# Kernel tuning notes

Measured on AMD Instinct MI355X. Metric: run time of the kernel, lower is better.

The kernel has to match this reference:

```python
import jax, jax.numpy as jnp
import numpy as np
from functools import partial

D_MODEL = 768
N_LAYER = 2
VOCAB = 50264  # 50257 padded to multiple of 8
D_STATE = 16
D_INNER = 2 * D_MODEL
DT_RANK = 48
D_CONV = 4
EPS = 1e-5
ZOH_EPS = 1e-7
B, L = 2, 1024


def setup_inputs() -> dict:
    key = jax.random.key(0)
    ks = jax.random.split(key, 16)
    s = 0.02
    inp = {
        'input_ids': jax.random.randint(ks[0], (B, L), 0, VOCAB, dtype=jnp.int32),
        'embedding': jax.random.normal(ks[1], (VOCAB, D_MODEL), jnp.float32) * s,
        'in_w': jax.random.normal(ks[2], (N_LAYER, D_MODEL, 2 * D_INNER), jnp.float32) * s,
        'in_b': jnp.zeros((N_LAYER, 2 * D_INNER), jnp.float32),
        'conv_w': jax.random.normal(ks[3], (N_LAYER, D_INNER, D_CONV), jnp.float32) * s,
        'conv_b': jnp.zeros((N_LAYER, D_INNER), jnp.float32),
        'xproj_w': jax.random.normal(ks[4], (N_LAYER, D_INNER, DT_RANK + 2 * D_STATE), jnp.float32) * s,
        'dt_w': jax.random.normal(ks[5], (N_LAYER, DT_RANK, D_INNER), jnp.float32) * s,
        'dt_b': jnp.zeros((N_LAYER, D_INNER), jnp.float32),
        'A_log': jnp.broadcast_to(jnp.log(jnp.arange(1, D_STATE + 1, dtype=jnp.float32))[None, None, :], (N_LAYER, D_INNER, D_STATE)).copy(),
        'Dp': jnp.ones((N_LAYER, D_INNER), jnp.float32),
        'out_w': jax.random.normal(ks[6], (N_LAYER, D_INNER, D_MODEL), jnp.float32) * s,
        'out_b': jnp.zeros((N_LAYER, D_MODEL), jnp.float32),
        'norm_w': jnp.ones((N_LAYER, D_MODEL), jnp.float32),
        'normf_w': jnp.ones((D_MODEL,), jnp.float32),
    }
    return inp


def rmsnorm(x, w):
    return x * jax.lax.rsqrt(jnp.mean(x * x, axis=-1, keepdims=True) + EPS) * w


def mamba_block(x, in_w, in_b, conv_w, conv_b, xproj_w, dt_w, dt_b, A_log, Dp, out_w, out_b):
    # x: (b, l, d_model)
    xr = x @ in_w + in_b                       # (b, l, 2*d_inner)
    xi, res = jnp.split(xr, 2, axis=-1)        # each (b, l, d_inner)
    # causal depthwise conv1d (torch pads d_conv-1 both sides then truncates to l)
    xc = jnp.transpose(xi, (0, 2, 1))          # (b, d_inner, l)
    xc = jax.lax.conv_general_dilated(
        xc, conv_w[:, None, :], (1,), [(D_CONV - 1, 0)],
        dimension_numbers=('NCH', 'OIH', 'NCH'), feature_group_count=D_INNER)
    xc = xc + conv_b[None, :, None]
    u = jax.nn.silu(jnp.transpose(xc, (0, 2, 1)))  # (b, l, d_inner)
    res = jax.nn.silu(res)
    # generate time-varying SSM params
    dbc = u @ xproj_w                          # (b, l, dt_rank + 2n)
    dt, Bm, Cm = jnp.split(dbc, [DT_RANK, DT_RANK + D_STATE], axis=-1)
    delta = jax.nn.softplus(dt @ dt_w + dt_b)  # (b, l, d_inner)
    A = -jnp.exp(A_log)                        # (d_inner, n)
    # ZOH discretization
    dA = jnp.exp(jnp.einsum('bld,dn->bldn', delta, A))            # (b,l,d_in,n)
    zoh = (dA - 1.0) / (A + ZOH_EPS)                               # (b,l,d_in,n)
    dBu = zoh * Bm[:, :, None, :] * u[..., None]                   # (b,l,d_in,n)
    # selective scan over l
    def step(s, inputs):
        dA_t, dBu_t, C_t = inputs              # (b,d_in,n),(b,d_in,n),(b,n)
        s = dA_t * s + dBu_t
        y = jnp.einsum('bdn,bn->bd', s, C_t)
        return s, y
    s0 = jnp.zeros((u.shape[0], D_INNER, D_STATE), u.dtype)
    _, ys = jax.lax.scan(step, s0, (jnp.moveaxis(dA, 1, 0), jnp.moveaxis(dBu, 1, 0), jnp.moveaxis(Cm, 1, 0)))
    y = jnp.moveaxis(ys, 0, 1) + u * Dp        # (b, l, d_inner)
    y = y * res
    return y @ out_w + out_b


def forward(input_ids, embedding, in_w, in_b, conv_w, conv_b, xproj_w, dt_w, dt_b, A_log, Dp, out_w, out_b, norm_w, normf_w):
    x = embedding[input_ids]                   # (b, l, d_model)
    for i in range(N_LAYER):
        mixed = mamba_block(x, in_w[i], in_b[i], conv_w[i], conv_b[i], xproj_w[i],
                            dt_w[i], dt_b[i], A_log[i], Dp[i], out_w[i], out_b[i])
        x = rmsnorm(mixed + x, norm_w[i])      # ResidualBlock: norm(mixer(x)+x)
    x = rmsnorm(x, normf_w)
    return x @ embedding.T                     # tied lm_head, (b, l, vocab)


def reference(input_ids, embedding, in_w, in_b, conv_w, conv_b, xproj_w, dt_w, dt_b, A_log, Dp, out_w, out_b, norm_w, normf_w):
    return forward(input_ids, embedding, in_w, in_b, conv_w, conv_b, xproj_w,
                   dt_w, dt_b, A_log, Dp, out_w, out_b, norm_w, normf_w)
```

## Files before the change

kernel.cpp:

```cpp
#include <hip/hip_runtime.h>
#include <math.h>
#include <stdint.h>

#define BB 2
#define LL 1024
#define DM 768
#define NL 2
#define VV 50264
#define VP2 50432
#define DS 16
#define DI 1536
#define DR 48
#define DC 4
#define MM (BB*LL)

#define CH 32
#define NC (LL/CH)

#define KS 8

#define TS 64
#define KT 16

typedef __attribute__((ext_vector_type(8))) short short8;
typedef __attribute__((ext_vector_type(4))) float f32x4;

#define AS3(p) ((__attribute__((address_space(3))) unsigned int*)(unsigned int)(uintptr_t)(p))
#define AS1(p) ((const __attribute__((address_space(1))) unsigned int*)(uintptr_t)(p))

__device__ __forceinline__ unsigned short f2bf(float v) {
    union { float f; unsigned u; } x; x.f = v;
    unsigned r = x.u + 0x7fffu + ((x.u >> 16) & 1u);
    return (unsigned short)(r >> 16);
}

__global__ __launch_bounds__(256) void embed_kernel(
    const int* __restrict__ ids, const float* __restrict__ emb,
    float* __restrict__ x, unsigned short* __restrict__ x16)
{
    int m = blockIdx.x;
    int v = ids[m];
    const float* src = emb + (size_t)v * DM;
    float* dst = x + (size_t)m * DM;
    unsigned short* dst16 = x16 + (size_t)m * DM;
    for (int i = threadIdx.x; i < DM; i += 256) {
        float f = src[i];
        dst[i] = f;
        dst16[i] = f2bf(f);
    }
}

__global__ __launch_bounds__(256) void emb_convert_kernel(
    const float* __restrict__ emb, unsigned short* __restrict__ out)
{
    size_t i8 = (size_t)blockIdx.x * 256 + threadIdx.x;
    size_t row = i8 / 96;
    size_t col8 = (i8 - row * 96) * 8;
    if (row >= VP2) return;
    ushort4 o0, o1;
    if (row < VV) {
        const float* p = emb + row * DM + col8;
        float4 v0 = *(const float4*)p;
        float4 v1 = *(const float4*)(p + 4);
        o0.x = f2bf(v0.x); o0.y = f2bf(v0.y); o0.z = f2bf(v0.z); o0.w = f2bf(v0.w);
        o1.x = f2bf(v1.x); o1.y = f2bf(v1.y); o1.z = f2bf(v1.z); o1.w = f2bf(v1.w);
    } else {
        o0 = make_ushort4(0, 0, 0, 0);
        o1 = o0;
    }
    unsigned short* op = out + row * DM + col8;
    *(ushort4*)op = o0;
    *(ushort4*)(op + 4) = o1;
}

__global__ __launch_bounds__(256) void transpose_bf16_kernel(
    const float* __restrict__ in, unsigned short* __restrict__ out, int R, int C)
{
    __shared__ float t[32][33];
    int l = blockIdx.z;
    int r0 = blockIdx.y * 32, c0 = blockIdx.x * 32;
    int tx = threadIdx.x & 31, ty = threadIdx.x >> 5;
    const float* ip = in + (size_t)l * R * C;
    unsigned short* op = out + (size_t)l * C * R;
    #pragma unroll
    for (int j = 0; j < 32; j += 8)
        t[ty + j][tx] = ip[(size_t)(r0 + ty + j) * C + c0 + tx];
    __syncthreads();
    #pragma unroll
    for (int j = 0; j < 32; j += 8)
        op[(size_t)(c0 + ty + j) * R + r0 + tx] = f2bf(t[tx][ty + j]);
}

__global__ __launch_bounds__(256) void gemm_mfma_bt(
    const unsigned short* __restrict__ A, const unsigned short* __restrict__ B,
    const float* __restrict__ bias, const float* __restrict__ resid,
    float* __restrict__ C, int M, int N, int K, int MT, int NTILES)
{
    int T = MT * NTILES;
    int q = T >> 3, r = T & 7;
    int orig = blockIdx.x;
    int xcd = orig & 7, u = orig >> 3;
    int wg = (xcd < r ? xcd * (q + 1) : r * (q + 1) + (xcd - r) * q) + u;
    int mt = wg % MT, nt = wg / MT;

    __shared__ unsigned short As[3][128 * 32];
    __shared__ unsigned short Bs[3][128 * 32];
    int tid = threadIdx.x;
    int w = tid >> 6, lane = tid & 63;
    int m0 = mt * 128, n0 = nt * 128;

    int rA = lane >> 2;
    int kb = (lane & 3) * 8;
    const unsigned short* gA0 = A + (size_t)(m0 + w * 16 + rA) * K + kb;
    const unsigned short* gA1 = gA0 + (size_t)64 * K;
    const unsigned short* gB0 = B + (size_t)(n0 + w * 16 + rA) * K + kb;
    const unsigned short* gB1 = gB0 + (size_t)64 * K;

    int lr = lane & 15, lk = lane >> 4;
    int wr = (w >> 1) * 64, wc = (w & 1) * 64;

    f32x4 acc[4][4] = {};

#define STAGE(k0, buf) do { \
    __builtin_amdgcn_global_load_lds(AS1(gA0 + (k0)), AS3(&As[buf][(w * 16) * 32]), 16, 0, 0); \
    __builtin_amdgcn_global_load_lds(AS1(gA1 + (k0)), AS3(&As[buf][(64 + w * 16) * 32]), 16, 0, 0); \
    __builtin_amdgcn_global_load_lds(AS1(gB0 + (k0)), AS3(&Bs[buf][(w * 16) * 32]), 16, 0, 0); \
    __builtin_amdgcn_global_load_lds(AS1(gB1 + (k0)), AS3(&Bs[buf][(64 + w * 16) * 32]), 16, 0, 0); \
} while (0)

#define COMPUTE(buf) do { \
    short8 a[4], b[4]; \
    _Pragma("unroll") \
    for (int f = 0; f < 4; ++f) \
        a[f] = *(const short8*)&As[buf][(wr + f * 16 + lr) * 32 + lk * 8]; \
    _Pragma("unroll") \
    for (int f = 0; f < 4; ++f) \
        b[f] = *(const short8*)&Bs[buf][(wc + f * 16 + lr) * 32 + lk * 8]; \
    _Pragma("unroll") \
    for (int i = 0; i < 4; ++i) \
        _Pragma("unroll") \
        for (int j = 0; j < 4; ++j) \
            acc[i][j] = __builtin_amdgcn_mfma_f32_16x16x32_bf16(a[i], b[j], acc[i][j], 0, 0, 0); \
} while (0)

    int nsteps = K / 32;
    STAGE(0, 0);
    STAGE(32, 1);
    asm volatile("s_waitcnt vmcnt(4)" ::: "memory");
    __builtin_amdgcn_s_barrier();
    __builtin_amdgcn_sched_barrier(0);

    for (int t = 0; t < nsteps; ++t) {
        int cur = t % 3;
        if (t + 2 < nsteps)
            STAGE((t + 2) * 32, (t + 2) % 3);
        COMPUTE(cur);
        if (t + 1 < nsteps) {
            if (t + 2 < nsteps)
                asm volatile("s_waitcnt vmcnt(4)" ::: "memory");
            else
                asm volatile("s_waitcnt vmcnt(0)" ::: "memory");
            __builtin_amdgcn_s_barrier();
            __builtin_amdgcn_sched_barrier(0);
        }
    }

#undef STAGE
#undef COMPUTE

    #pragma unroll
    for (int i = 0; i < 4; ++i) {
        int row = m0 + wr + i * 16 + lk * 4;
        #pragma unroll
        for (int j = 0; j < 4; ++j) {
            int col = n0 + wc + j * 16 + lr;
            if (col < N) {
                float bv = bias ? bias[col] : 0.f;
                #pragma unroll
                for (int r2 = 0; r2 < 4; ++r2) {
                    float v = acc[i][j][r2] + bv;
                    if (resid) v += resid[(size_t)(row + r2) * N + col];
                    C[(size_t)(row + r2) * N + col] = v;
                }
            }
        }
    }
}

__global__ __launch_bounds__(512) void gemm_mfma_256(
    const unsigned short* __restrict__ A, const unsigned short* __restrict__ B,
    float* __restrict__ C, int M, int N, int K, int MT, int NTILES)
{
    int T = MT * NTILES;
    int q = T >> 3, r = T & 7;
    int orig = blockIdx.x;
    int xcd = orig & 7, u = orig >> 3;
    int wg = (xcd < r ? xcd * (q + 1) : r * (q + 1) + (xcd - r) * q) + u;
    int mt = wg % MT, nt = wg / MT;

    __shared__ unsigned short As[3][256 * 32];
    __shared__ unsigned short Bs[3][256 * 32];
    int tid = threadIdx.x;
    int w = tid >> 6, lane = tid & 63;
    int wm = w >> 2, wn = w & 3;
    int m0 = mt * 256, n0 = nt * 256;

    int srow = tid >> 2;
    int schunk = (tid & 3) ^ ((srow & 3) ^ ((srow >> 2) & 3));
    const unsigned short* gA0 = A + (size_t)(m0 + srow) * K + schunk * 8;
    const unsigned short* gA1 = gA0 + (size_t)128 * K;
    const unsigned short* gB0 = B + (size_t)(n0 + srow) * K + schunk * 8;
    const unsigned short* gB1 = gB0 + (size_t)128 * K;

    int lr = lane & 15, lk = lane >> 4;
    int rc = (lk ^ ((lr & 3) ^ ((lr >> 2) & 3))) * 8;

    f32x4 acc[8][4] = {};

#define STAGE_A(k0, buf) do { \
    __builtin_amdgcn_global_load_lds(AS1(gA0 + (k0)), AS3(&As[buf][(w * 16) * 32]), 16, 0, 0); \
    __builtin_amdgcn_global_load_lds(AS1(gA1 + (k0)), AS3(&As[buf][(128 + w * 16) * 32]), 16, 0, 0); \
} while (0)
#define STAGE_B(k0, buf) do { \
    __builtin_amdgcn_global_load_lds(AS1(gB0 + (k0)), AS3(&Bs[buf][(w * 16) * 32]), 16, 0, 0); \
    __builtin_amdgcn_global_load_lds(AS1(gB1 + (k0)), AS3(&Bs[buf][(128 + w * 16) * 32]), 16, 0, 0); \
} while (0)

    int nsteps = K / 32;

    STAGE_A(0, 0); STAGE_B(0, 0);
    STAGE_A(32, 1); STAGE_B(32, 1);
    asm volatile("s_waitcnt vmcnt(4)" ::: "memory");
    __builtin_amdgcn_s_barrier();
    __builtin_amdgcn_sched_barrier(0);

    for (int t = 0; t < nsteps; ++t) {
        int s = t % 3;
        int sn = (t + 2) % 3;
        bool stage2 = (t + 2) < nsteps;
        short8 av[4], bv[4];

        #pragma unroll
        for (int f = 0; f < 4; ++f)
            av[f] = *(const short8*)&As[s][(wm * 128 + f * 16 + lr) * 32 + rc];
        #pragma unroll
        for (int f = 0; f < 4; ++f)
            bv[f] = *(const short8*)&Bs[s][(wn * 64 + f * 16 + lr) * 32 + rc];
        if (stage2) STAGE_A((t + 2) * 32, sn);
        __builtin_amdgcn_s_barrier();
        asm volatile("s_waitcnt lgkmcnt(0)" ::: "memory");
        __builtin_amdgcn_sched_barrier(0);
        __builtin_amdgcn_s_setprio(1);
        #pragma unroll
        for (int i = 0; i < 4; ++i)
            #pragma unroll
            for (int j = 0; j < 4; ++j)
                acc[i][j] = __builtin_amdgcn_mfma_f32_16x16x32_bf16(av[i], bv[j], acc[i][j], 0, 0, 0);
        __builtin_amdgcn_s_setprio(0);
        __builtin_amdgcn_s_barrier();

        #pragma unroll
        for (int f = 0; f < 4; ++f)
            av[f] = *(const short8*)&As[s][(wm * 128 + (4 + f) * 16 + lr) * 32 + rc];
        if (stage2) STAGE_B((t + 2) * 32, sn);
        __builtin_amdgcn_s_barrier();
        asm volatile("s_waitcnt lgkmcnt(0)" ::: "memory");
        __builtin_amdgcn_sched_barrier(0);
        __builtin_amdgcn_s_setprio(1);
        #pragma unroll
        for (int i = 0; i < 4; ++i)
            #pragma unroll
            for (int j = 0; j < 4; ++j)
                acc[4 + i][j] = __builtin_amdgcn_mfma_f32_16x16x32_bf16(av[i], bv[j], acc[4 + i][j], 0, 0, 0);
        __builtin_amdgcn_s_setprio(0);

        if (t + 1 < nsteps) {
            if (stage2)
                asm volatile("s_waitcnt vmcnt(4)" ::: "memory");
            else
                asm volatile("s_waitcnt vmcnt(0)" ::: "memory");
            __builtin_amdgcn_s_barrier();
            __builtin_amdgcn_sched_barrier(0);
        }
    }

#undef STAGE_A
#undef STAGE_B

    #pragma unroll
    for (int i = 0; i < 8; ++i) {
        int row = m0 + wm * 128 + i * 16 + lk * 4;
        #pragma unroll
        for (int j = 0; j < 4; ++j) {
            int col = n0 + wn * 64 + j * 16 + lr;
            if (col < N) {
                #pragma unroll
                for (int r2 = 0; r2 < 4; ++r2)
                    C[(size_t)(row + r2) * N + col] = acc[i][j][r2];
            }
        }
    }
}

template<int ACT>
__global__ __launch_bounds__(256) void gemm_tiled(
    const float* __restrict__ A, const float* __restrict__ Bm,
    const float* __restrict__ bias, float* __restrict__ C,
    int M, int N, int K, int lda)
{
    __shared__ float As[KT][TS + 4];
    __shared__ float Bs[KT][TS + 4];
    int tid = threadIdx.x;
    int tx = tid & 15, ty = tid >> 4;
    int m0 = blockIdx.y * TS;
    int n0 = blockIdx.x * TS;
    float acc[4][4] = {};

    for (int k0 = 0; k0 < K; k0 += KT) {
        {
            int i = tid >> 2;
            int k4 = (tid & 3) * 4;
            int m = m0 + i;
            float4 v = make_float4(0.f, 0.f, 0.f, 0.f);
            if (m < M) v = *(const float4*)(A + (size_t)m * lda + k0 + k4);
            As[k4 + 0][i] = v.x; As[k4 + 1][i] = v.y;
            As[k4 + 2][i] = v.z; As[k4 + 3][i] = v.w;
        }
        {
            int k = tid >> 4;
            int j4 = (tid & 15) * 4;
            int n = n0 + j4;
            float4 v = make_float4(0.f, 0.f, 0.f, 0.f);
            const float* p = Bm + (size_t)(k0 + k) * N + n;
            if (n + 3 < N) {
                v = *(const float4*)p;
            } else {
                float t0 = (n + 0 < N) ? p[0] : 0.f;
                float t1 = (n + 1 < N) ? p[1] : 0.f;
                float t2 = (n + 2 < N) ? p[2] : 0.f;
                float t3 = (n + 3 < N) ? p[3] : 0.f;
                v = make_float4(t0, t1, t2, t3);
            }
            Bs[k][j4 + 0] = v.x; Bs[k][j4 + 1] = v.y;
            Bs[k][j4 + 2] = v.z; Bs[k][j4 + 3] = v.w;
        }
        __syncthreads();
        #pragma unroll
        for (int k = 0; k < KT; ++k) {
            float a[4], b[4];
            #pragma unroll
            for (int q2 = 0; q2 < 4; ++q2) a[q2] = As[k][ty * 4 + q2];
            #pragma unroll
            for (int q2 = 0; q2 < 4; ++q2) b[q2] = Bs[k][tx * 4 + q2];
            #pragma unroll
            for (int i = 0; i < 4; ++i)
                #pragma unroll
                for (int j = 0; j < 4; ++j)
                    acc[i][j] = fmaf(a[i], b[j], acc[i][j]);
        }
        __syncthreads();
    }

    #pragma unroll
    for (int i = 0; i < 4; ++i) {
        int m = m0 + ty * 4 + i;
        if (m >= M) continue;
        #pragma unroll
        for (int j = 0; j < 4; ++j) {
            int n = n0 + tx * 4 + j;
            if (n >= N) continue;
            float v = acc[i][j];
            if (bias)  v += bias[n];
            if (ACT == 1) v = fmaxf(v, 0.f) + log1pf(expf(-fabsf(v)));
            C[(size_t)m * N + n] = v;
        }
    }
}

__global__ __launch_bounds__(256) void xproj_part_kernel(
    const float* __restrict__ A, const float* __restrict__ Bm, float* __restrict__ part)
{
    __shared__ float As[KT][TS + 4];
    __shared__ float Bs[KT][TS + 4];
    int tid = threadIdx.x;
    int tx = tid & 15, ty = tid >> 4;
    int m0 = blockIdx.y * TS;
    int n0 = blockIdx.x * TS;
    int kbeg = blockIdx.z * (DI / KS);
    const int N = 80;
    float acc[4][4] = {};

    for (int k0 = kbeg; k0 < kbeg + DI / KS; k0 += KT) {
        {
            int i = tid >> 2;
            int k4 = (tid & 3) * 4;
            float4 v = *(const float4*)(A + (size_t)(m0 + i) * DI + k0 + k4);
            As[k4 + 0][i] = v.x; As[k4 + 1][i] = v.y;
            As[k4 + 2][i] = v.z; As[k4 + 3][i] = v.w;
        }
        {
            int k = tid >> 4;
            int j4 = (tid & 15) * 4;
            int n = n0 + j4;
            const float* p = Bm + (size_t)(k0 + k) * N + n;
            float4 v;
            if (n + 3 < N) {
                v = *(const float4*)p;
            } else {
                v.x = (n + 0 < N) ? p[0] : 0.f;
                v.y = (n + 1 < N) ? p[1] : 0.f;
                v.z = (n + 2 < N) ? p[2] : 0.f;
                v.w = (n + 3 < N) ? p[3] : 0.f;
            }
            Bs[k][j4 + 0] = v.x; Bs[k][j4 + 1] = v.y;
            Bs[k][j4 + 2] = v.z; Bs[k][j4 + 3] = v.w;
        }
        __syncthreads();
        #pragma unroll
        for (int k = 0; k < KT; ++k) {
            float a[4], b[4];
            #pragma unroll
            for (int q2 = 0; q2 < 4; ++q2) a[q2] = As[k][ty * 4 + q2];
            #pragma unroll
            for (int q2 = 0; q2 < 4; ++q2) b[q2] = Bs[k][tx * 4 + q2];
            #pragma unroll
            for (int i = 0; i < 4; ++i)
                #pragma unroll
                for (int j = 0; j < 4; ++j)
                    acc[i][j] = fmaf(a[i], b[j], acc[i][j]);
        }
        __syncthreads();
    }

    float* op = part + (size_t)blockIdx.z * MM * 80;
    #pragma unroll
    for (int i = 0; i < 4; ++i) {
        int m = m0 + ty * 4 + i;
        #pragma unroll
        for (int j = 0; j < 4; ++j) {
            int n = n0 + tx * 4 + j;
            if (n < 80) op[(size_t)m * 80 + n] = acc[i][j];
        }
    }
}

__global__ __launch_bounds__(256) void xproj_reduce_kernel(
    const float* __restrict__ part, float* __restrict__ dbc)
{
    int i = blockIdx.x * 256 + threadIdx.x;
    if (i >= MM * 80) return;
    float s = 0.f;
    #pragma unroll
    for (int z = 0; z < KS; ++z) s += part[(size_t)z * MM * 80 + i];
    dbc[i] = s;
}

__global__ __launch_bounds__(256) void conv_silu_kernel(
    const float* __restrict__ xr, const float* __restrict__ cw,
    const float* __restrict__ cb, float* __restrict__ u)
{
    int d = blockIdx.x * 256 + threadIdx.x;
    int l = blockIdx.y;
    int b = blockIdx.z;
    float acc = cb[d];
    #pragma unroll
    for (int j = 0; j < DC; ++j) {
        int lp = l - (DC - 1) + j;
        if (lp >= 0)
            acc = fmaf(xr[((size_t)(b * LL + lp)) * (2 * DI) + d], cw[d * DC + j], acc);
    }
    float s = acc / (1.f + expf(-acc));
    u[((size_t)(b * LL + l)) * DI + d] = s;
}

__global__ __launch_bounds__(256) void scan_reduce_kernel(
    const float* __restrict__ delta, const float* __restrict__ u,
    const float* __restrict__ dbc, const float* __restrict__ A_log,
    float* __restrict__ P, float* __restrict__ Q)
{
    int d = blockIdx.x * 256 + threadIdx.x;
    int c = blockIdx.y;
    int b = blockIdx.z;

    float Av[DS], invA[DS];
    {
        const float4* ap = (const float4*)(A_log + (size_t)d * DS);
        #pragma unroll
        for (int n4 = 0; n4 < 4; ++n4) {
            float4 a = ap[n4];
            Av[n4 * 4 + 0] = -expf(a.x); Av[n4 * 4 + 1] = -expf(a.y);
            Av[n4 * 4 + 2] = -expf(a.z); Av[n4 * 4 + 3] = -expf(a.w);
        }
        #pragma unroll
        for (int n = 0; n < DS; ++n) invA[n] = 1.f / (Av[n] + 1e-7f);
    }

    float p[DS], s[DS];
    #pragma unroll
    for (int n = 0; n < DS; ++n) { p[n] = 1.f; s[n] = 0.f; }

    const float* dp = delta + ((size_t)b * LL + c * CH) * DI + d;
    const float* up = u     + ((size_t)b * LL + c * CH) * DI + d;
    const float* bb = dbc   + ((size_t)b * LL + c * CH) * 80 + DR;

    for (int l = 0; l < CH; ++l) {
        float dlt = dp[(size_t)l * DI];
        float uv  = up[(size_t)l * DI];
        float Bv[DS];
        {
            const float4* bp4 = (const float4*)(bb + (size_t)l * 80);
            #pragma unroll
            for (int n4 = 0; n4 < 4; ++n4) {
                float4 v = bp4[n4];
                Bv[n4 * 4 + 0] = v.x; Bv[n4 * 4 + 1] = v.y;
                Bv[n4 * 4 + 2] = v.z; Bv[n4 * 4 + 3] = v.w;
            }
        }
        #pragma unroll
        for (int n = 0; n < DS; ++n) {
            float dA = expf(dlt * Av[n]);
            float dBu = (dA - 1.f) * invA[n] * Bv[n] * uv;
            p[n] *= dA;
            s[n] = fmaf(dA, s[n], dBu);
        }
    }

    float* Pp = P + (((size_t)b * NC + c) * DI + d) * DS;
    float* Qp = Q + (((size_t)b * NC + c) * DI + d) * DS;
    #pragma unroll
    for (int n4 = 0; n4 < 4; ++n4) {
        ((float4*)Pp)[n4] = make_float4(p[n4 * 4 + 0], p[n4 * 4 + 1], p[n4 * 4 + 2], p[n4 * 4 + 3]);
        ((float4*)Qp)[n4] = make_float4(s[n4 * 4 + 0], s[n4 * 4 + 1], s[n4 * 4 + 2], s[n4 * 4 + 3]);
    }
}

__global__ __launch_bounds__(256) void scan_apply_kernel(
    const float* __restrict__ delta, const float* __restrict__ u,
    const float* __restrict__ dbc, const float* __restrict__ xr,
    const float* __restrict__ A_log, const float* __restrict__ Dp,
    const float* __restrict__ P, const float* __restrict__ Q,
    unsigned short* __restrict__ y16)
{
    int d = blockIdx.x * 256 + threadIdx.x;
    int c = blockIdx.y;
    int b = blockIdx.z;

    float Av[DS], invA[DS];
    {
        const float4* ap = (const float4*)(A_log + (size_t)d * DS);
        #pragma unroll
        for (int n4 = 0; n4 < 4; ++n4) {
            float4 a = ap[n4];
            Av[n4 * 4 + 0] = -expf(a.x); Av[n4 * 4 + 1] = -expf(a.y);
            Av[n4 * 4 + 2] = -expf(a.z); Av[n4 * 4 + 3] = -expf(a.w);
        }
        #pragma unroll
        for (int n = 0; n < DS; ++n) invA[n] = 1.f / (Av[n] + 1e-7f);
    }
    float Dv = Dp[d];

    float s[DS];
    #pragma unroll
    for (int n = 0; n < DS; ++n) s[n] = 0.f;
    for (int cc = 0; cc < c; ++cc) {
        const float* Pp = P + (((size_t)b * NC + cc) * DI + d) * DS;
        const float* Qp = Q + (((size_t)b * NC + cc) * DI + d) * DS;
        float pv[DS], qv[DS];
        #pragma unroll
        for (int n4 = 0; n4 < 4; ++n4) {
            float4 pw = ((const float4*)Pp)[n4];
            float4 qw = ((const float4*)Qp)[n4];
            pv[n4 * 4 + 0] = pw.x; pv[n4 * 4 + 1] = pw.y; pv[n4 * 4 + 2] = pw.z; pv[n4 * 4 + 3] = pw.w;
            qv[n4 * 4 + 0] = qw.x; qv[n4 * 4 + 1] = qw.y; qv[n4 * 4 + 2] = qw.z; qv[n4 * 4 + 3] = qw.w;
        }
        #pragma unroll
        for (int n = 0; n < DS; ++n) s[n] = fmaf(pv[n], s[n], qv[n]);
    }

    const float* dp = delta + ((size_t)b * LL + c * CH) * DI + d;
    const float* up = u     + ((size_t)b * LL + c * CH) * DI + d;
    const float* xp = xr    + ((size_t)b * LL + c * CH) * (2 * DI) + DI + d;
    const float* bb = dbc   + ((size_t)b * LL + c * CH) * 80 + DR;
    unsigned short* yp = y16 + ((size_t)b * LL + c * CH) * DI + d;

    for (int l = 0; l < CH; ++l) {
        float dlt = dp[(size_t)l * DI];
        float uv  = up[(size_t)l * DI];
        float rv  = xp[(size_t)l * (2 * DI)];
        float Bv[DS], Cv[DS];
        {
            const float4* bp4 = (const float4*)(bb + (size_t)l * 80);
            #pragma unroll
            for (int n4 = 0; n4 < 4; ++n4) {
                float4 v = bp4[n4];
                Bv[n4 * 4 + 0] = v.x; Bv[n4 * 4 + 1] = v.y;
                Bv[n4 * 4 + 2] = v.z; Bv[n4 * 4 + 3] = v.w;
            }
            #pragma unroll
            for (int n4 = 0; n4 < 4; ++n4) {
                float4 v = bp4[4 + n4];
                Cv[n4 * 4 + 0] = v.x; Cv[n4 * 4 + 1] = v.y;
                Cv[n4 * 4 + 2] = v.z; Cv[n4 * 4 + 3] = v.w;
            }
        }
        float pv = 0.f;
        #pragma unroll
        for (int n = 0; n < DS; ++n) {
            float dA = expf(dlt * Av[n]);
            float dBu = (dA - 1.f) * invA[n] * Bv[n] * uv;
            s[n] = fmaf(dA, s[n], dBu);
            pv = fmaf(s[n], Cv[n], pv);
        }
        float res = rv / (1.f + expf(-rv));
        yp[(size_t)l * DI] = f2bf((pv + uv * Dv) * res);
    }
}

__global__ __launch_bounds__(256) void rmsnorm_kernel(
    const float* __restrict__ in, const float* __restrict__ w,
    float* __restrict__ outf, unsigned short* __restrict__ outb)
{
    int m = blockIdx.x;
    const float* row = in + (size_t)m * DM;
    float ss = 0.f;
    for (int i = threadIdx.x; i < DM; i += 256) { float v = row[i]; ss = fmaf(v, v, ss); }
    #pragma unroll
    for (int off = 32; off > 0; off >>= 1) ss += __shfl_down(ss, off);
    __shared__ float sred[4];
    __shared__ float sscale;
    int wid = threadIdx.x >> 6;
    if ((threadIdx.x & 63) == 0) sred[wid] = ss;
    __syncthreads();
    if (threadIdx.x == 0) {
        float tot = sred[0] + sred[1] + sred[2] + sred[3];
        sscale = 1.f / sqrtf(tot / (float)DM + 1e-5f);
    }
    __syncthreads();
    float sc = sscale;
    for (int i = threadIdx.x; i < DM; i += 256) {
        float v = row[i] * sc * w[i];
        if (outf) outf[(size_t)m * DM + i] = v;
        if (outb) outb[(size_t)m * DM + i] = f2bf(v);
    }
}

extern "C" void kernel_launch(void* const* d_in, const int* in_sizes, int n_in,
                              void* d_out, int out_size, void* d_ws, size_t ws_size,
                              hipStream_t stream)
{
    const int*   ids      = (const int*)  d_in[0];
    const float* emb      = (const float*)d_in[1];
    const float* in_w     = (const float*)d_in[2];
    const float* in_b     = (const float*)d_in[3];
    const float* conv_w   = (const float*)d_in[4];
    const float* conv_b   = (const float*)d_in[5];
    const float* xproj_w  = (const float*)d_in[6];
    const float* dt_w     = (const float*)d_in[7];
    const float* dt_b     = (const float*)d_in[8];
    const float* A_log    = (const float*)d_in[9];
    const float* Dp       = (const float*)d_in[10];
    const float* out_w    = (const float*)d_in[11];
    const float* out_b    = (const float*)d_in[12];
    const float* norm_w   = (const float*)d_in[13];
    const float* normf_w  = (const float*)d_in[14];
    float* out = (float*)d_out;

    char* wsp = (char*)d_ws;
    auto alloc = [&](size_t bytes) {
        char* p = wsp;
        wsp += (bytes + 255) & ~(size_t)255;
        return p;
    };
    float* x     = (float*)alloc((size_t)MM * DM * 4);
    float* xr    = (float*)alloc((size_t)MM * 2 * DI * 4);
    float* u     = (float*)alloc((size_t)MM * DI * 4);
    float* dbc   = (float*)alloc((size_t)MM * 80 * 4);
    float* part  = (float*)alloc((size_t)KS * MM * 80 * 4);
    float* delta = (float*)alloc((size_t)MM * DI * 4);
    float* tmp   = (float*)alloc((size_t)MM * DM * 4);
    float* Pbuf  = (float*)alloc((size_t)BB * NC * DI * DS * 4);
    float* Qbuf  = (float*)alloc((size_t)BB * NC * DI * DS * 4);
    unsigned short* x16     = (unsigned short*)alloc((size_t)MM * DM * 2);
    unsigned short* y16     = (unsigned short*)alloc((size_t)MM * DI * 2);
    unsigned short* emb16   = (unsigned short*)alloc((size_t)VP2 * DM * 2);
    unsigned short* in_wT   = (unsigned short*)alloc((size_t)NL * 2 * DI * DM * 2);
    unsigned short* out_wT  = (unsigned short*)alloc((size_t)NL * DM * DI * 2);

    emb_convert_kernel<<<((size_t)VP2 * (DM / 8) + 255) / 256, 256, 0, stream>>>(emb, emb16);
    transpose_bf16_kernel<<<dim3(2 * DI / 32, DM / 32, NL), 256, 0, stream>>>(
        in_w, in_wT, DM, 2 * DI);
    transpose_bf16_kernel<<<dim3(DM / 32, DI / 32, NL), 256, 0, stream>>>(
        out_w, out_wT, DI, DM);

    embed_kernel<<<MM, 256, 0, stream>>>(ids, emb, x, x16);

    for (int layer = 0; layer < NL; ++layer) {
        const float* lb_in  = in_b    + (size_t)layer * 2 * DI;
        const float* lcw    = conv_w  + (size_t)layer * DI * DC;
        const float* lcb    = conv_b  + (size_t)layer * DI;
        const float* lxw    = xproj_w + (size_t)layer * DI * (DR + 2 * DS);
        const float* ldtw   = dt_w    + (size_t)layer * DR * DI;
        const float* ldtb   = dt_b    + (size_t)layer * DI;
        const float* lAlog  = A_log   + (size_t)layer * DI * DS;
        const float* lDp    = Dp      + (size_t)layer * DI;
        const float* lob    = out_b   + (size_t)layer * DM;
        const float* lnw    = norm_w  + (size_t)layer * DM;
        const unsigned short* lw_inT = in_wT  + (size_t)layer * 2 * DI * DM;
        const unsigned short* lw_outT= out_wT + (size_t)layer * DM * DI;

        gemm_mfma_bt<<<16 * 24, 256, 0, stream>>>(
            x16, lw_inT, lb_in, nullptr, xr, MM, 2 * DI, DM, 16, 24);

        conv_silu_kernel<<<dim3(DI / 256, LL, BB), 256, 0, stream>>>(xr, lcw, lcb, u);

        xproj_part_kernel<<<dim3(2, MM / TS, KS), 256, 0, stream>>>(u, lxw, part);
        xproj_reduce_kernel<<<(MM * 80 + 255) / 256, 256, 0, stream>>>(part, dbc);

        gemm_tiled<1><<<dim3(DI / TS, MM / TS), 256, 0, stream>>>(
            dbc, ldtw, ldtb, delta, MM, DI, DR, DR + 2 * DS);

        scan_reduce_kernel<<<dim3(DI / 256, NC, BB), 256, 0, stream>>>(
            delta, u, dbc, lAlog, Pbuf, Qbuf);
        scan_apply_kernel<<<dim3(DI / 256, NC, BB), 256, 0, stream>>>(
            delta, u, dbc, xr, lAlog, lDp, Pbuf, Qbuf, y16);

        gemm_mfma_bt<<<16 * 6, 256, 0, stream>>>(
            y16, lw_outT, lob, x, tmp, MM, DM, DI, 16, 6);

        rmsnorm_kernel<<<MM, 256, 0, stream>>>(tmp, lnw, x, x16);
    }

    rmsnorm_kernel<<<MM, 256, 0, stream>>>(x, normf_w, nullptr, x16);

    gemm_mfma_256<<<8 * (VP2 / 256), 512, 0, stream>>>(
        x16, emb16, out, MM, VV, DM, 8, VP2 / 256);
}
```

Before: 810.9 us.

## Fuse fp32-to-bf16 embedding conversion into lm_head GEMM B-operand staging

Removes the separate emb_convert_kernel that wrote a full bf16 copy of the embedding table. The lm_head GEMM now loads fp32 embedding rows into registers, converts them to bf16 and writes them into swizzled shared memory itself, and loads for later steps are issued ahead so they overlap the MFMA work. This saves one full pass over the 154MB table plus the bf16 write and re-read. In exchange, each of the 8 M-tiles re-reads and re-converts fp32 B (twice the bytes of bf16), and the register-staged path replaces the direct global-to-LDS loads, which may weaken pipelining.

```diff
diff --git a/kernel.cpp b/kernel.cpp
--- a/kernel.cpp
+++ b/kernel.cpp
@@ -48,29 +48,6 @@
         dst[i] = f;
         dst16[i] = f2bf(f);
     }
-}
-
-__global__ __launch_bounds__(256) void emb_convert_kernel(
-    const float* __restrict__ emb, unsigned short* __restrict__ out)
-{
-    size_t i8 = (size_t)blockIdx.x * 256 + threadIdx.x;
-    size_t row = i8 / 96;
-    size_t col8 = (i8 - row * 96) * 8;
-    if (row >= VP2) return;
-    ushort4 o0, o1;
-    if (row < VV) {
-        const float* p = emb + row * DM + col8;
-        float4 v0 = *(const float4*)p;
-        float4 v1 = *(const float4*)(p + 4);
-        o0.x = f2bf(v0.x); o0.y = f2bf(v0.y); o0.z = f2bf(v0.z); o0.w = f2bf(v0.w);
-        o1.x = f2bf(v1.x); o1.y = f2bf(v1.y); o1.z = f2bf(v1.z); o1.w = f2bf(v1.w);
-    } else {
-        o0 = make_ushort4(0, 0, 0, 0);
-        o1 = o0;
-    }
-    unsigned short* op = out + row * DM + col8;
-    *(ushort4*)op = o0;
-    *(ushort4*)(op + 4) = o1;
 }
 
 __global__ __launch_bounds__(256) void transpose_bf16_kernel(
@@ -188,7 +165,7 @@
 }
 
 __global__ __launch_bounds__(512) void gemm_mfma_256(
-    const unsigned short* __restrict__ A, const unsigned short* __restrict__ B,
+    const unsigned short* __restrict__ A, const float* __restrict__ Bf,
     float* __restrict__ C, int M, int N, int K, int MT, int NTILES)
 {
     int T = MT * NTILES;
@@ -209,8 +186,15 @@
     int schunk = (tid & 3) ^ ((srow & 3) ^ ((srow >> 2) & 3));
     const unsigned short* gA0 = A + (size_t)(m0 + srow) * K + schunk * 8;
     const unsigned short* gA1 = gA0 + (size_t)128 * K;
-    const unsigned short* gB0 = B + (size_t)(n0 + srow) * K + schunk * 8;
-    const unsigned short* gB1 = gB0 + (size_t)128 * K;
+
+    int brow = tid >> 1;
+    int bh = tid & 1;
+    int growR = n0 + brow;
+    bool bvalid = growR < VV;
+    const float* gBf = Bf + (size_t)(bvalid ? growR : (VV - 1)) * K + bh * 16;
+    int sgB = (brow & 3) ^ ((brow >> 2) & 3);
+    int cB0 = (2 * bh) ^ sgB;
+    int cB1 = (2 * bh + 1) ^ sgB;
 
     int lr = lane & 15, lk = lane >> 4;
     int rc = (lk ^ ((lr & 3) ^ ((lr >> 2) & 3))) * 8;
@@ -221,22 +205,48 @@
     __builtin_amdgcn_global_load_lds(AS1(gA0 + (k0)), AS3(&As[buf][(w * 16) * 32]), 16, 0, 0); \
     __builtin_amdgcn_global_load_lds(AS1(gA1 + (k0)), AS3(&As[buf][(128 + w * 16) * 32]), 16, 0, 0); \
 } while (0)
-#define STAGE_B(k0, buf) do { \
-    __builtin_amdgcn_global_load_lds(AS1(gB0 + (k0)), AS3(&Bs[buf][(w * 16) * 32]), 16, 0, 0); \
-    __builtin_amdgcn_global_load_lds(AS1(gB1 + (k0)), AS3(&Bs[buf][(128 + w * 16) * 32]), 16, 0, 0); \
+
+#define BCONVERT_WRITE(slot) do { \
+    if (!bvalid) { q0 = make_float4(0,0,0,0); q1 = q0; q2 = q0; q3 = q0; } \
+    uint4 p0, p1; \
+    p0.x = (unsigned)f2bf(q0.x) | ((unsigned)f2bf(q0.y) << 16); \
+    p0.y = (unsigned)f2bf(q0.z) | ((unsigned)f2bf(q0.w) << 16); \
+    p0.z = (unsigned)f2bf(q1.x) | ((unsigned)f2bf(q1.y) << 16); \
+    p0.w = (unsigned)f2bf(q1.z) | ((unsigned)f2bf(q1.w) << 16); \
+    p1.x = (unsigned)f2bf(q2.x) | ((unsigned)f2bf(q2.y) << 16); \
+    p1.y = (unsigned)f2bf(q2.z) | ((unsigned)f2bf(q2.w) << 16); \
+    p1.z = (unsigned)f2bf(q3.x) | ((unsigned)f2bf(q3.y) << 16); \
+    p1.w = (unsigned)f2bf(q3.z) | ((unsigned)f2bf(q3.w) << 16); \
+    *(uint4*)&Bs[slot][brow * 32 + cB0 * 8] = p0; \
+    *(uint4*)&Bs[slot][brow * 32 + cB1 * 8] = p1; \
 } while (0)
 
     int nsteps = K / 32;
-
-    STAGE_A(0, 0); STAGE_B(0, 0);
-    STAGE_A(32, 1); STAGE_B(32, 1);
+    float4 q0, q1, q2, q3;
+
+    q0 = *(const float4*)(gBf + 0);
+    q1 = *(const float4*)(gBf + 4);
+    q2 = *(const float4*)(gBf + 8);
+    q3 = *(const float4*)(gBf + 12);
+    __builtin_amdgcn_sched_barrier(0);
+    STAGE_A(0, 0);
+    STAGE_A(32, 1);
+    __builtin_amdgcn_sched_barrier(0);
     asm volatile("s_waitcnt vmcnt(4)" ::: "memory");
+    BCONVERT_WRITE(0);
+    q0 = *(const float4*)(gBf + 32 + 0);
+    q1 = *(const float4*)(gBf + 32 + 4);
+    q2 = *(const float4*)(gBf + 32 + 8);
+    q3 = *(const float4*)(gBf + 32 + 12);
+    __builtin_amdgcn_sched_barrier(0);
+    asm volatile("s_waitcnt vmcnt(6) lgkmcnt(0)" ::: "memory");
     __builtin_amdgcn_s_barrier();
     __builtin_amdgcn_sched_barrier(0);
 
     for (int t = 0; t < nsteps; ++t) {
         int s = t % 3;
         int sn = (t + 2) % 3;
+        bool haveB = (t + 1) < nsteps;
         bool stage2 = (t + 2) < nsteps;
         short8 av[4], bv[4];
 
@@ -262,7 +272,6 @@
         #pragma unroll
         for (int f = 0; f < 4; ++f)
             av[f] = *(const short8*)&As[s][(wm * 128 + (4 + f) * 16 + lr) * 32 + rc];
-        if (stage2) STAGE_B((t + 2) * 32, sn);
         __builtin_amdgcn_s_barrier();
         asm volatile("s_waitcnt lgkmcnt(0)" ::: "memory");
         __builtin_amdgcn_sched_barrier(0);
@@ -274,18 +283,30 @@
                 acc[4 + i][j] = __builtin_amdgcn_mfma_f32_16x16x32_bf16(av[i], bv[j], acc[4 + i][j], 0, 0, 0);
         __builtin_amdgcn_s_setprio(0);
 
-        if (t + 1 < nsteps) {
+        if (haveB) {
             if (stage2)
-                asm volatile("s_waitcnt vmcnt(4)" ::: "memory");
+                asm volatile("s_waitcnt vmcnt(2)" ::: "memory");
             else
                 asm volatile("s_waitcnt vmcnt(0)" ::: "memory");
+            BCONVERT_WRITE((t + 1) % 3);
+            if (t + 2 < nsteps) {
+                q0 = *(const float4*)(gBf + (t + 2) * 32 + 0);
+                q1 = *(const float4*)(gBf + (t + 2) * 32 + 4);
+                q2 = *(const float4*)(gBf + (t + 2) * 32 + 8);
+                q3 = *(const float4*)(gBf + (t + 2) * 32 + 12);
+            }
+            __builtin_amdgcn_sched_barrier(0);
+        }
+
+        if (t + 1 < nsteps) {
+            asm volatile("s_waitcnt lgkmcnt(0)" ::: "memory");
             __builtin_amdgcn_s_barrier();
             __builtin_amdgcn_sched_barrier(0);
         }
     }
 
 #undef STAGE_A
-#undef STAGE_B
+#undef BCONVERT_WRITE
 
     #pragma unroll
     for (int i = 0; i < 8; ++i) {
@@ -682,11 +703,9 @@
     float* Qbuf  = (float*)alloc((size_t)BB * NC * DI * DS * 4);
     unsigned short* x16     = (unsigned short*)alloc((size_t)MM * DM * 2);
     unsigned short* y16     = (unsigned short*)alloc((size_t)MM * DI * 2);
-    unsigned short* emb16   = (unsigned short*)alloc((size_t)VP2 * DM * 2);
     unsigned short* in_wT   = (unsigned short*)alloc((size_t)NL * 2 * DI * DM * 2);
     unsigned short* out_wT  = (unsigned short*)alloc((size_t)NL * DM * DI * 2);
 
-    emb_convert_kernel<<<((size_t)VP2 * (DM / 8) + 255) / 256, 256, 0, stream>>>(emb, emb16);
     transpose_bf16_kernel<<<dim3(2 * DI / 32, DM / 32, NL), 256, 0, stream>>>(
         in_w, in_wT, DM, 2 * DI);
     transpose_bf16_kernel<<<dim3(DM / 32, DI / 32, NL), 256, 0, stream>>>(
@@ -733,5 +752,5 @@
     rmsnorm_kernel<<<MM, 256, 0, stream>>>(x, normf_w, nullptr, x16);
 
     gemm_mfma_256<<<8 * (VP2 / 256), 512, 0, stream>>>(
-        x16, emb16, out, MM, VV, DM, 8, VP2 / 256);
-}
+        x16, emb, out, MM, VV, DM, 8, VP2 / 256);
+}
```

Measured after the change: 838.9 us. +3.4%, slower.
